# Kernel tuning notes

Measured on AMD Instinct MI355X. Metric: run time of the kernel, lower is better.

Reference implementation:

```python
import jax, jax.numpy as jnp
import numpy as np

HIDDEN = 768
N_HEADS = 12
HEAD_DIM = HIDDEN // N_HEADS  # 64 (multihead=True)
NEG_BIG = -1e31


def setup_inputs() -> dict:
    key = jax.random.key(0)
    ks = jax.random.split(key, 8)
    B, S = 4, 2048
    toks = jax.random.normal(ks[0], (B, S, HIDDEN), dtype=jnp.float32)
    masks = jax.random.randint(ks[1], (B, S), 0, 2, dtype=jnp.int32)
    s = 0.02
    Wq = jax.random.normal(ks[2], (HIDDEN, HIDDEN), dtype=jnp.float32) * s
    Wk = jax.random.normal(ks[3], (HIDDEN, HIDDEN), dtype=jnp.float32) * s
    Wv = jax.random.normal(ks[4], (HIDDEN, HIDDEN), dtype=jnp.float32) * s
    bq = jax.random.normal(ks[5], (HIDDEN,), dtype=jnp.float32) * s
    bk = jax.random.normal(ks[6], (HIDDEN,), dtype=jnp.float32) * s
    bv = jax.random.normal(ks[7], (HIDDEN,), dtype=jnp.float32) * s
    return {"toks": toks, "masks": masks, "Wq": Wq, "bq": bq,
            "Wk": Wk, "bk": bk, "Wv": Wv, "bv": bv}


def reference(toks, masks, Wq, bq, Wk, bk, Wv, bv):
    B, S, D = toks.shape
    m = masks.astype(jnp.float32)  # [B,S]
    # additive outer-product padding mask: (1 - m_i*m_j) * -1e31, shape [B,S,S]
    add_mask = (1.0 - m[:, :, None] * m[:, None, :]) * NEG_BIG

    def split_heads(x):  # [B,S,D] -> [B,H,S,hd]
        return x.reshape(B, S, N_HEADS, HEAD_DIM).transpose(0, 2, 1, 3)

    q = split_heads(toks @ Wq + bq)
    k = split_heads(toks @ Wk + bk)
    v = split_heads(toks @ Wv + bv)

    scores = jnp.einsum("bhqd,bhkd->bhqk", q, k) / jnp.sqrt(
        jnp.asarray(HEAD_DIM, dtype=toks.dtype))
    scores = scores + add_mask[:, None, :, :]
    probs = jax.nn.softmax(scores, axis=-1)  # dropout is identity at eval
    ctx = jnp.einsum("bhqk,bhkd->bhqd", probs, v)
    return ctx.transpose(0, 2, 1, 3).reshape(B, S, D)
```

## Files before the change

kernel.cpp:

```cpp
#include <hip/hip_runtime.h>
#include <hip/hip_bf16.h>
#include <cstddef>


typedef __bf16 bf16_8 __attribute__((ext_vector_type(8)));
typedef float f32x4 __attribute__((ext_vector_type(4)));
typedef short s16x4 __attribute__((ext_vector_type(4)));
typedef short s16x8 __attribute__((ext_vector_type(8)));

#define HID 768
#define NHEADS 12
#define HD 64
#define BATCH 4
#define SEQ 2048
#define NEGBIG2 (-1.44269504e31f)
#define SCALE2 0.18033688f

#define KT 64
#define NKT (SEQ / KT)
#define STR 68
#define ASTR 40

static __device__ __forceinline__ f32x4 mfma16x16x32(bf16_8 a, bf16_8 b, f32x4 c) {
  return __builtin_amdgcn_mfma_f32_16x16x32_bf16(a, b, c, 0, 0, 0);
}

static __device__ __forceinline__ void lds_barrier() {
  __asm__ volatile("s_waitcnt lgkmcnt(0)\n\ts_barrier" ::: "memory");
}

static __device__ __forceinline__ float fast_exp2(float x) {
#if __has_builtin(__builtin_amdgcn_exp2f)
  return __builtin_amdgcn_exp2f(x);
#else
  return __expf(x * 0.69314718f);
#endif
}

static __device__ __forceinline__ s16x4 pack_bf16x4(f32x4 p) {
  s16x4 o;
#pragma unroll
  for (int i = 0; i < 4; ++i) {
    __bf16 b = (__bf16)p[i];
    o[i] = __builtin_bit_cast(short, b);
  }
  return o;
}

static __device__ __forceinline__ bf16_8 cat2(const __bf16* p) {
  s16x4 lo = *(const s16x4*)p;
  s16x4 hi = *(const s16x4*)(p + 4);
  s16x8 v = __builtin_shufflevector(lo, hi, 0, 1, 2, 3, 4, 5, 6, 7);
  return __builtin_bit_cast(bf16_8, v);
}

static __device__ __forceinline__ void write2(__bf16* p, s16x8 v) {
  *(s16x4*)p = __builtin_shufflevector(v, v, 0, 1, 2, 3);
  *(s16x4*)(p + 4) = __builtin_shufflevector(v, v, 4, 5, 6, 7);
}

static __device__ __forceinline__ bf16_8 cvt_a_frag(const float* p) {
  f32x4 af0 = *(const f32x4*)p;
  f32x4 af1 = *(const f32x4*)(p + 4);
  bf16_8 a;
  a[0] = (__bf16)af0[0]; a[1] = (__bf16)af0[1];
  a[2] = (__bf16)af0[2]; a[3] = (__bf16)af0[3];
  a[4] = (__bf16)af1[0]; a[5] = (__bf16)af1[1];
  a[6] = (__bf16)af1[2]; a[7] = (__bf16)af1[3];
  return a;
}

__global__ __launch_bounds__(256) void mask_kadd(const int* __restrict__ masks,
                                                 float* __restrict__ kaddG) {
  int i = blockIdx.x * 256 + threadIdx.x;
  kaddG[i] = masks[i] ? 0.0f : NEGBIG2;
}

__global__ __launch_bounds__(256) void transpose768x3(const float* __restrict__ Wq,
                                                      const float* __restrict__ Wk,
                                                      const float* __restrict__ Wv,
                                                      __bf16* __restrict__ WtBase) {
  const float* in = blockIdx.z == 0 ? Wq : (blockIdx.z == 1 ? Wk : Wv);
  __bf16* out = WtBase + (size_t)blockIdx.z * HID * HID;
  __shared__ __bf16 tile[32][33];
  int bx = blockIdx.x * 32, by = blockIdx.y * 32;
  int tx = threadIdx.x, ty = threadIdx.y;
#pragma unroll
  for (int r = 0; r < 32; r += 8)
    tile[ty + r][tx] = (__bf16)in[(size_t)(by + ty + r) * HID + bx + tx];
  __syncthreads();
#pragma unroll
  for (int r = 0; r < 32; r += 8)
    out[(size_t)(bx + ty + r) * HID + by + tx] = tile[tx][ty + r];
}

__global__ __launch_bounds__(256, 4) void proj_kv(const float* __restrict__ toks,
                                                  const __bf16* __restrict__ WtK,
                                                  const float* __restrict__ bk,
                                                  const __bf16* __restrict__ WtV,
                                                  const float* __restrict__ bv,
                                                  __bf16* __restrict__ Kout,
                                                  __bf16* __restrict__ Vtout,
                                                  int head0, int hm) {
  __shared__ __align__(16) __bf16 ldsA[2][64 * ASTR];
  int tid = threadIdx.x;
  int w = tid >> 6, lane = tid & 63, l16 = lane & 15, quad = lane >> 4;
  int m0 = blockIdx.x * 64;
  int hl = blockIdx.y, h = head0 + hl;
  int srow = tid >> 2, scg = tid & 3;
  const float* asrc = toks + (size_t)(m0 + srow) * HID + scg * 8;
  const __bf16* bKrow = WtK + (size_t)(h * 64 + w * 16 + l16) * HID + quad * 8;
  const __bf16* bVrow = WtV + (size_t)(h * 64 + w * 16 + l16) * HID + quad * 8;
  f32x4 zero = {0.f, 0.f, 0.f, 0.f};
  f32x4 aK[4], aV[4];
#pragma unroll
  for (int mt = 0; mt < 4; ++mt) { aK[mt] = zero; aV[mt] = zero; }

  *(bf16_8*)(&ldsA[0][srow * ASTR + scg * 8]) = cvt_a_frag(asrc);
  __syncthreads();

  const int NCH = HID / 32;
  for (int t = 0; t < NCH; ++t) {
    int b = t & 1;
    int kk = t * 32;
    bf16_8 areg;
    if (t + 1 < NCH) areg = cvt_a_frag(asrc + kk + 32);
    bf16_8 bkf = *(const bf16_8*)(bKrow + kk);
    bf16_8 bvf = *(const bf16_8*)(bVrow + kk);
#pragma unroll
    for (int mt = 0; mt < 4; ++mt) {
      bf16_8 af = *(const bf16_8*)(&ldsA[b][(mt * 16 + l16) * ASTR + quad * 8]);
      aK[mt] = mfma16x16x32(af, bkf, aK[mt]);
      aV[mt] = mfma16x16x32(af, bvf, aV[mt]);
    }
    if (t + 1 < NCH) {
      *(bf16_8*)(&ldsA[b ^ 1][srow * ASTR + scg * 8]) = areg;
      lds_barrier();
    }
  }

  int d = w * 16 + l16;
  float bnK = bk[h * 64 + d];
  float bnV = bv[h * 64 + d];
#pragma unroll
  for (int mt = 0; mt < 4; ++mt) {
#pragma unroll
    for (int r = 0; r < 4; ++r) {
      int m = m0 + mt * 16 + quad * 4 + r;
      int b = m >> 11;
      int s = m & (SEQ - 1);
      Kout[(((size_t)b * hm + hl) * SEQ + s) * HD + d] = (__bf16)(aK[mt][r] + bnK);
      Vtout[(((size_t)b * hm + hl) * HD + d) * SEQ + s] = (__bf16)(aV[mt][r] + bnV);
    }
  }
}

__global__ __launch_bounds__(256, 3) void attn_fused(const float* __restrict__ toks,
                                                     const __bf16* __restrict__ WtQ,
                                                     const float* __restrict__ bq,
                                                     const __bf16* __restrict__ Kbuf,
                                                     const __bf16* __restrict__ Vtbuf,
                                                     const float* __restrict__ kaddG,
                                                     float* __restrict__ out,
                                                     int head0, int hm) {
  __shared__ __align__(16) __bf16 ldsK[2][64 * STR];
  __shared__ __align__(16) __bf16 ldsV[2][64 * STR];
  __shared__ __align__(16) __bf16 ldsQP[64 * STR];
  int tid = threadIdx.x;
  int w = tid >> 6, lane = tid & 63, l16 = lane & 15, quad = lane >> 4;
  int bz = blockIdx.z, hl = blockIdx.y, h = head0 + hl;
  int q0 = blockIdx.x * 64;
  const float* kb = kaddG + (size_t)bz * SEQ;
  f32x4 zero = {0.f, 0.f, 0.f, 0.f};

  const __bf16* Kb = Kbuf + ((size_t)bz * hm + hl) * SEQ * HD;
  const __bf16* Vb = Vtbuf + ((size_t)bz * hm + hl) * HD * SEQ;

  {
    const float* arow = toks + ((size_t)bz * SEQ + q0 + w * 16 + l16) * HID + quad * 8;
    const __bf16* brow = WtQ + (size_t)(h * 64 + l16) * HID + quad * 8;
    f32x4 qa[4] = {zero, zero, zero, zero};
    for (int kk = 0; kk < HID; kk += 32) {
      bf16_8 a = cvt_a_frag(arow + kk);
#pragma unroll
      for (int t = 0; t < 4; ++t)
        qa[t] = mfma16x16x32(a, *(const bf16_8*)(brow + (size_t)t * 16 * HID + kk), qa[t]);
    }
#pragma unroll
    for (int t = 0; t < 4; ++t) {
      float bn = bq[h * 64 + t * 16 + l16];
#pragma unroll
      for (int r = 0; r < 4; ++r)
        ldsQP[(w * 16 + quad * 4 + r) * STR + t * 16 + l16] = (__bf16)(qa[t][r] + bn);
    }
  }

  int srow = tid >> 3, sc = tid & 7;
  {
    s16x8 k0 = *(const s16x8*)(Kb + (size_t)srow * HD + sc * 8);
    s16x8 k1 = *(const s16x8*)(Kb + (size_t)(srow + 32) * HD + sc * 8);
    s16x8 v0 = *(const s16x8*)(Vb + (size_t)srow * SEQ + sc * 8);
    s16x8 v1 = *(const s16x8*)(Vb + (size_t)(srow + 32) * SEQ + sc * 8);
    write2(&ldsK[0][srow * STR + sc * 8], k0);
    write2(&ldsK[0][(srow + 32) * STR + sc * 8], k1);
    write2(&ldsV[0][srow * STR + sc * 8], v0);
    write2(&ldsV[0][(srow + 32) * STR + sc * 8], v1);
  }
  __syncthreads();

  bf16_8 qf[4][2];
#pragma unroll
  for (int s = 0; s < 4; ++s)
#pragma unroll
    for (int half = 0; half < 2; ++half)
      qf[s][half] = cat2(&ldsQP[(s * 16 + l16) * STR + half * 32 + quad * 8]);
  float actq[4];
#pragma unroll
  for (int s = 0; s < 4; ++s) actq[s] = (kb[q0 + s * 16 + l16] == 0.0f) ? 1.0f : 0.0f;
  __syncthreads();

  float lsum[4] = {0.f, 0.f, 0.f, 0.f};
  f32x4 acc[4];
#pragma unroll
  for (int s = 0; s < 4; ++s) acc[s] = zero;

  for (int t = 0; t < NKT; ++t) {
    int j0 = t * KT;
    int jn = (t + 1 < NKT) ? j0 + KT : 0;
    int buf = t & 1, nbuf = buf ^ 1;
    s16x8 k0 = *(const s16x8*)(Kb + (size_t)(jn + srow) * HD + sc * 8);
    s16x8 k1 = *(const s16x8*)(Kb + (size_t)(jn + srow + 32) * HD + sc * 8);
    s16x8 v0 = *(const s16x8*)(Vb + (size_t)srow * SEQ + jn + sc * 8);
    s16x8 v1 = *(const s16x8*)(Vb + (size_t)(srow + 32) * SEQ + jn + sc * 8);

    bf16_8 kf0 = cat2(&ldsK[buf][(w * 16 + l16) * STR + quad * 8]);
    bf16_8 kf1 = cat2(&ldsK[buf][(w * 16 + l16) * STR + 32 + quad * 8]);
    f32x4 ck = *(const f32x4*)(kb + j0 + w * 16 + quad * 4);
#pragma unroll
    for (int s = 0; s < 4; ++s) {
      f32x4 st = mfma16x16x32(kf1, qf[s][1], mfma16x16x32(kf0, qf[s][0], zero));
      f32x4 p;
#pragma unroll
      for (int r = 0; r < 4; ++r) {
        float v = actq[s] * fmaf(st[r], SCALE2, ck[r]);
        p[r] = fast_exp2(v);
      }
      lsum[s] += p[0] + p[1] + p[2] + p[3];
      *(s16x4*)(&ldsQP[(s * 16 + l16) * STR + w * 16 + quad * 4]) = pack_bf16x4(p);
    }
    lds_barrier();

#pragma unroll
    for (int kc = 0; kc < 2; ++kc) {
      bf16_8 vf = cat2(&ldsV[buf][(w * 16 + l16) * STR + kc * 32 + quad * 8]);
#pragma unroll
      for (int s = 0; s < 4; ++s) {
        bf16_8 pf = cat2(&ldsQP[(s * 16 + l16) * STR + kc * 32 + quad * 8]);
        acc[s] = mfma16x16x32(pf, vf, acc[s]);
      }
    }
    write2(&ldsK[nbuf][srow * STR + sc * 8], k0);
    write2(&ldsK[nbuf][(srow + 32) * STR + sc * 8], k1);
    write2(&ldsV[nbuf][srow * STR + sc * 8], v0);
    write2(&ldsV[nbuf][(srow + 32) * STR + sc * 8], v1);
    lds_barrier();
  }

  __syncthreads();
  float* ls = (float*)ldsQP;
#pragma unroll
  for (int s = 0; s < 4; ++s) {
    float v = lsum[s];
    v += __shfl_xor(v, 16);
    v += __shfl_xor(v, 32);
    if (quad == 0) ls[(w * 4 + s) * 16 + l16] = v;
  }
  __syncthreads();
  float lr[4][4];
#pragma unroll
  for (int s = 0; s < 4; ++s) {
    float tot = ls[(0 * 4 + s) * 16 + l16] + ls[(1 * 4 + s) * 16 + l16] +
                ls[(2 * 4 + s) * 16 + l16] + ls[(3 * 4 + s) * 16 + l16];
    float linv = 1.0f / tot;
#pragma unroll
    for (int r = 0; r < 4; ++r) lr[s][r] = __shfl(linv, quad * 4 + r);
  }
#pragma unroll
  for (int s = 0; s < 4; ++s)
#pragma unroll
    for (int r = 0; r < 4; ++r)
      out[((size_t)bz * SEQ + q0 + s * 16 + quad * 4 + r) * HID + h * HD + w * 16 + l16] =
          acc[s][r] * lr[s][r];
}

extern "C" void kernel_launch(void* const* d_in, const int* in_sizes, int n_in,
                              void* d_out, int out_size, void* d_ws, size_t ws_size,
                              hipStream_t stream) {
  (void)in_sizes; (void)n_in; (void)out_size;
  const float* toks = (const float*)d_in[0];
  const int* masks = (const int*)d_in[1];
  const float* Wq = (const float*)d_in[2];
  const float* bq = (const float*)d_in[3];
  const float* Wk = (const float*)d_in[4];
  const float* bk = (const float*)d_in[5];
  const float* Wv = (const float*)d_in[6];
  const float* bv = (const float*)d_in[7];
  char* ws = (char*)d_ws;
  const size_t KADD_B = (size_t)BATCH * SEQ * 4;
  const size_t WT_B = (size_t)HID * HID * 2;
  const size_t KV_FULL_B = (size_t)BATCH * NHEADS * SEQ * HD * 2;
  const size_t KV_HEAD_B = (size_t)BATCH * SEQ * HD * 2;
  const size_t TIER_A_NEED = KADD_B + 3 * WT_B + 2 * KV_FULL_B;
  float* kaddG = (float*)(ws);
  __bf16* WtQ = (__bf16*)(ws + KADD_B + 0 * WT_B);
  __bf16* WtK = (__bf16*)(ws + KADD_B + 1 * WT_B);
  __bf16* WtV = (__bf16*)(ws + KADD_B + 2 * WT_B);
  float* outp = (float*)d_out;

  mask_kadd<<<BATCH * SEQ / 256, 256, 0, stream>>>(masks, kaddG);
  dim3 tgrid(HID / 32, HID / 32, 3), tblk(32, 8);
  transpose768x3<<<tgrid, tblk, 0, stream>>>(Wq, Wk, Wv, WtQ);

  if (ws_size >= TIER_A_NEED) {
    __bf16* Kf = (__bf16*)(ws + KADD_B + 3 * WT_B);
    __bf16* Vtf = (__bf16*)(ws + KADD_B + 3 * WT_B + KV_FULL_B);
    dim3 pgrid(BATCH * SEQ / 64, NHEADS);
    proj_kv<<<pgrid, 256, 0, stream>>>(toks, WtK, bk, WtV, bv, Kf, Vtf, 0, NHEADS);
    dim3 agrid(SEQ / 64, NHEADS, BATCH);
    attn_fused<<<agrid, 256, 0, stream>>>(toks, WtQ, bq, Kf, Vtf, kaddG, outp, 0, NHEADS);
  } else {
    __bf16* Kh = (__bf16*)(ws + KADD_B + 3 * WT_B);
    __bf16* Vth = (__bf16*)(ws + KADD_B + 3 * WT_B + KV_HEAD_B);
    dim3 pgrid(BATCH * SEQ / 64, 1);
    dim3 agrid(SEQ / 64, 1, BATCH);
    for (int h = 0; h < NHEADS; ++h) {
      proj_kv<<<pgrid, 256, 0, stream>>>(toks, WtK, bk, WtV, bv, Kh, Vth, h, 1);
      attn_fused<<<agrid, 256, 0, stream>>>(toks, WtQ, bq, Kh, Vth, kaddG, outp, h, 1);
    }
  }
}
```

Baseline: 305.6 us.

## Load K and V fragments directly from global into registers, drop LDS staging

K and V tiles are now loaded straight from global memory into the MFMA operand registers each wave needs, instead of being staged cooperatively through double-buffered LDS. Only the P tile stays in LDS, now double-buffered, which removes the second barrier per iteration. The smaller LDS footprint allows raising the occupancy hint from 3 to 4 blocks per CU. In exchange each wave issues its own global loads for K/V with less cross-wave reuse, which relies on L1/L2 caching, and the V loads are issued in the same iteration that uses them, so their latency is not prefetched.

```diff
diff --git a/kernel.cpp b/kernel.cpp
--- a/kernel.cpp
+++ b/kernel.cpp
@@ -155,7 +155,7 @@
   }
 }
 
-__global__ __launch_bounds__(256, 3) void attn_fused(const float* __restrict__ toks,
+__global__ __launch_bounds__(256, 4) void attn_fused(const float* __restrict__ toks,
                                                      const __bf16* __restrict__ WtQ,
                                                      const float* __restrict__ bq,
                                                      const __bf16* __restrict__ Kbuf,
@@ -163,9 +163,7 @@
                                                      const float* __restrict__ kaddG,
                                                      float* __restrict__ out,
                                                      int head0, int hm) {
-  __shared__ __align__(16) __bf16 ldsK[2][64 * STR];
-  __shared__ __align__(16) __bf16 ldsV[2][64 * STR];
-  __shared__ __align__(16) __bf16 ldsQP[64 * STR];
+  __shared__ __align__(16) __bf16 ldsP[2][64 * STR];
   int tid = threadIdx.x;
   int w = tid >> 6, lane = tid & 63, l16 = lane & 15, quad = lane >> 4;
   int bz = blockIdx.z, hl = blockIdx.y, h = head0 + hl;
@@ -191,20 +189,8 @@
       float bn = bq[h * 64 + t * 16 + l16];
 #pragma unroll
       for (int r = 0; r < 4; ++r)
-        ldsQP[(w * 16 + quad * 4 + r) * STR + t * 16 + l16] = (__bf16)(qa[t][r] + bn);
-    }
-  }
-
-  int srow = tid >> 3, sc = tid & 7;
-  {
-    s16x8 k0 = *(const s16x8*)(Kb + (size_t)srow * HD + sc * 8);
-    s16x8 k1 = *(const s16x8*)(Kb + (size_t)(srow + 32) * HD + sc * 8);
-    s16x8 v0 = *(const s16x8*)(Vb + (size_t)srow * SEQ + sc * 8);
-    s16x8 v1 = *(const s16x8*)(Vb + (size_t)(srow + 32) * SEQ + sc * 8);
-    write2(&ldsK[0][srow * STR + sc * 8], k0);
-    write2(&ldsK[0][(srow + 32) * STR + sc * 8], k1);
-    write2(&ldsV[0][srow * STR + sc * 8], v0);
-    write2(&ldsV[0][(srow + 32) * STR + sc * 8], v1);
+        ldsP[0][(w * 16 + quad * 4 + r) * STR + t * 16 + l16] = (__bf16)(qa[t][r] + bn);
+    }
   }
   __syncthreads();
 
@@ -213,7 +199,7 @@
   for (int s = 0; s < 4; ++s)
 #pragma unroll
     for (int half = 0; half < 2; ++half)
-      qf[s][half] = cat2(&ldsQP[(s * 16 + l16) * STR + half * 32 + quad * 8]);
+      qf[s][half] = cat2(&ldsP[0][(s * 16 + l16) * STR + half * 32 + quad * 8]);
   float actq[4];
 #pragma unroll
   for (int s = 0; s < 4; ++s) actq[s] = (kb[q0 + s * 16 + l16] == 0.0f) ? 1.0f : 0.0f;
@@ -223,51 +209,55 @@
   f32x4 acc[4];
 #pragma unroll
   for (int s = 0; s < 4; ++s) acc[s] = zero;
+
+  const __bf16* kRow = Kb + (size_t)(w * 16 + l16) * HD + quad * 8;
+  const __bf16* vRow = Vb + (size_t)(w * 16 + l16) * SEQ + quad * 8;
+  const float* ckB = kb + w * 16 + quad * 4;
+
+  s16x8 kcur0 = *(const s16x8*)(kRow);
+  s16x8 kcur1 = *(const s16x8*)(kRow + 32);
+  f32x4 ckcur = *(const f32x4*)(ckB);
 
   for (int t = 0; t < NKT; ++t) {
     int j0 = t * KT;
     int jn = (t + 1 < NKT) ? j0 + KT : 0;
-    int buf = t & 1, nbuf = buf ^ 1;
-    s16x8 k0 = *(const s16x8*)(Kb + (size_t)(jn + srow) * HD + sc * 8);
-    s16x8 k1 = *(const s16x8*)(Kb + (size_t)(jn + srow + 32) * HD + sc * 8);
-    s16x8 v0 = *(const s16x8*)(Vb + (size_t)srow * SEQ + jn + sc * 8);
-    s16x8 v1 = *(const s16x8*)(Vb + (size_t)(srow + 32) * SEQ + jn + sc * 8);
-
-    bf16_8 kf0 = cat2(&ldsK[buf][(w * 16 + l16) * STR + quad * 8]);
-    bf16_8 kf1 = cat2(&ldsK[buf][(w * 16 + l16) * STR + 32 + quad * 8]);
-    f32x4 ck = *(const f32x4*)(kb + j0 + w * 16 + quad * 4);
+    int buf = t & 1;
+    s16x8 knxt0 = *(const s16x8*)(kRow + (size_t)jn * HD);
+    s16x8 knxt1 = *(const s16x8*)(kRow + (size_t)jn * HD + 32);
+    f32x4 cknxt = *(const f32x4*)(ckB + jn);
+    s16x8 vraw0 = *(const s16x8*)(vRow + j0);
+    s16x8 vraw1 = *(const s16x8*)(vRow + j0 + 32);
+
+    bf16_8 kfa = __builtin_bit_cast(bf16_8, kcur0);
+    bf16_8 kfb = __builtin_bit_cast(bf16_8, kcur1);
 #pragma unroll
     for (int s = 0; s < 4; ++s) {
-      f32x4 st = mfma16x16x32(kf1, qf[s][1], mfma16x16x32(kf0, qf[s][0], zero));
+      f32x4 st = mfma16x16x32(kfb, qf[s][1], mfma16x16x32(kfa, qf[s][0], zero));
       f32x4 p;
 #pragma unroll
       for (int r = 0; r < 4; ++r) {
-        float v = actq[s] * fmaf(st[r], SCALE2, ck[r]);
+        float v = actq[s] * fmaf(st[r], SCALE2, ckcur[r]);
         p[r] = fast_exp2(v);
       }
       lsum[s] += p[0] + p[1] + p[2] + p[3];
-      *(s16x4*)(&ldsQP[(s * 16 + l16) * STR + w * 16 + quad * 4]) = pack_bf16x4(p);
+      *(s16x4*)(&ldsP[buf][(s * 16 + l16) * STR + w * 16 + quad * 4]) = pack_bf16x4(p);
     }
     lds_barrier();
 
 #pragma unroll
     for (int kc = 0; kc < 2; ++kc) {
-      bf16_8 vf = cat2(&ldsV[buf][(w * 16 + l16) * STR + kc * 32 + quad * 8]);
+      bf16_8 vfr = __builtin_bit_cast(bf16_8, kc ? vraw1 : vraw0);
 #pragma unroll
       for (int s = 0; s < 4; ++s) {
-        bf16_8 pf = cat2(&ldsQP[(s * 16 + l16) * STR + kc * 32 + quad * 8]);
-        acc[s] = mfma16x16x32(pf, vf, acc[s]);
+        bf16_8 pf = cat2(&ldsP[buf][(s * 16 + l16) * STR + kc * 32 + quad * 8]);
+        acc[s] = mfma16x16x32(pf, vfr, acc[s]);
       }
     }
-    write2(&ldsK[nbuf][srow * STR + sc * 8], k0);
-    write2(&ldsK[nbuf][(srow + 32) * STR + sc * 8], k1);
-    write2(&ldsV[nbuf][srow * STR + sc * 8], v0);
-    write2(&ldsV[nbuf][(srow + 32) * STR + sc * 8], v1);
-    lds_barrier();
-  }
-
-  __syncthreads();
-  float* ls = (float*)ldsQP;
+    kcur0 = knxt0; kcur1 = knxt1; ckcur = cknxt;
+  }
+
+  __syncthreads();
+  float* ls = (float*)ldsP;
 #pragma unroll
   for (int s = 0; s < 4; ++s) {
     float v = lsum[s];
```

After: 326.6 us. +6.9%, slower.
